# Optimization experiments

Measured on AMD Instinct MI355X. Metric: run time of the kernel, lower is better.

Reference implementation:

```python
import jax, jax.numpy as jnp
import numpy as np

EPS = 1e-5


def bin_act(x):
    # forward of Binaryactivation: sign (STE backward handled in fwdbwd module)
    return jnp.sign(x)


def bin_conv(x, w, stride, padding):
    # per-output-filter scaling factor = mean |w| over (in, kh, kw), detached
    scale = jax.lax.stop_gradient(jnp.mean(jnp.abs(w), axis=(1, 2, 3), keepdims=True))
    bw = scale * jnp.sign(w)
    rw = jnp.clip(w, -1.0, 1.0)
    # STE blend: forward uses binary weight, backward flows through clamp(w)
    filt = jax.lax.stop_gradient(bw - rw) + rw
    return jax.lax.conv_general_dilated(
        x, filt, window_strides=(stride, stride),
        padding=[(padding, padding), (padding, padding)],
        dimension_numbers=("NCHW", "OIHW", "NCHW"))


def batchnorm(x, gamma, beta):
    # training-mode BN: biased batch stats over (N, H, W)
    mean = jnp.mean(x, axis=(0, 2, 3), keepdims=True)
    var = jnp.mean((x - mean) ** 2, axis=(0, 2, 3), keepdims=True)
    xn = (x - mean) * jax.lax.rsqrt(var + EPS)
    return xn * gamma[None, :, None, None] + beta[None, :, None, None]


def prelu(x, a):
    a = a[None, :, None, None]
    return jnp.where(x >= 0, x, a * x)


def addbias(x, b):
    return x + b[None, :, None, None]


def setup_inputs() -> dict:
    key = jax.random.key(0)
    ks = jax.random.split(key, 4)
    C = 256
    x = jax.random.normal(ks[0], (32, C, 56, 56), dtype=jnp.float32)
    # BinaryConv weights init: uniform[0, 0.001)
    w3x3 = jax.random.uniform(ks[1], (C, C, 3, 3), dtype=jnp.float32) * 0.001
    wres = jax.random.uniform(ks[2], (C, C, 1, 1), dtype=jnp.float32) * 0.001
    zeros = jnp.zeros((C,), dtype=jnp.float32)
    ones = jnp.ones((C,), dtype=jnp.float32)
    prelu_init = jnp.full((C,), 0.25, dtype=jnp.float32)
    return {
        "x": x,
        "b1_1": zeros, "w3x3": w3x3, "bn1_g": ones, "bn1_b": zeros,
        "b1_2": zeros, "prelu1_a": prelu_init, "b1_3": zeros,
        "b2_1": zeros, "wres": wres, "bn2_g": ones, "bn2_b": zeros,
        "b2_2": zeros, "prelu2_a": prelu_init, "b2_3": zeros,
    }


def reference(x, b1_1, w3x3, bn1_g, bn1_b, b1_2, prelu1_a, b1_3,
              b2_1, wres, bn2_g, bn2_b, b2_2, prelu2_a, b2_3):
    # branch 1: bias -> sign -> binary 3x3 conv -> BN -> residual add
    x1 = bin_act(addbias(x, b1_1))
    x1 = bin_conv(x1, w3x3, stride=1, padding=1)
    x1 = batchnorm(x1, bn1_g, bn1_b)
    x = x + x1
    x = addbias(x, b1_2)
    x = prelu(x, prelu1_a)
    x = addbias(x, b1_3)
    # branch 2 (in_channel == out_channel): binary 1x1 conv residual
    x2 = bin_act(addbias(x, b2_1))
    x2 = bin_conv(x2, wres, stride=1, padding=0)
    x2 = batchnorm(x2, bn2_g, bn2_b)
    x2 = x2 + x
    x2 = addbias(x2, b2_2)
    x2 = prelu(x2, prelu2_a)
    x2 = addbias(x2, b2_3)
    return x2
```

## Files before the change

### kernel.cpp

```cpp
#include <hip/hip_runtime.h>
#include <cstdint>
#include <math.h>

#define HW    3136
#define NPIX  100352
#define NELEM 25690112

#define OFF_PW1   0u
#define OFF_PW2   73728u
#define OFF_CORR  81920u
#define OFF_SC1   86016u
#define OFF_SC2   87040u
#define OFF_A1    88064u
#define OFF_B1    89088u
#define OFF_A2    90112u
#define OFF_B2    91136u
#define OFF_ST    92160u
#define ST_BYTES  524288u
#define OFF_P1    616448u
#define OFF_P2    3827712u
#define OFF_S1    7038976u
#define OFF_S2    58419200u

__global__ __launch_bounds__(256) void prep_w_k(const float* __restrict__ w3,
                         const float* __restrict__ wr,
                         uint32_t* __restrict__ pw1, uint32_t* __restrict__ pw2,
                         float* __restrict__ sc1, float* __restrict__ sc2,
                         short* __restrict__ corrG) {
  __shared__ float s1S[4], s2S[4];
  __shared__ int cntS[9][4];
  const int o = blockIdx.x;
  const int tid = threadIdx.x;
  const int l = tid & 63, wv = tid >> 6;
  const float* wo = w3 + (size_t)o * 2304 + (size_t)tid * 9;
  float w9[9];
#pragma unroll
  for (int t = 0; t < 9; ++t) w9[t] = wo[t];
  float s = 0.f;
#pragma unroll
  for (int t = 0; t < 9; ++t) s += fabsf(w9[t]);
#pragma unroll
  for (int m = 32; m; m >>= 1) s += __shfl_xor(s, m, 64);
#pragma unroll
  for (int t = 0; t < 9; ++t) {
    unsigned long long mb = __ballot(w9[t] >= 0.0f);
    if (l == 0) {
      pw1[(size_t)(o * 9 + t) * 8 + wv * 2 + 0] = (uint32_t)mb;
      pw1[(size_t)(o * 9 + t) * 8 + wv * 2 + 1] = (uint32_t)(mb >> 32);
      cntS[t][wv] = __popcll(mb);
    }
  }
  float v2 = wr[(size_t)o * 256 + tid];
  float s2 = fabsf(v2);
#pragma unroll
  for (int m = 32; m; m >>= 1) s2 += __shfl_xor(s2, m, 64);
  unsigned long long mb2 = __ballot(v2 >= 0.0f);
  if (l == 0) {
    pw2[(size_t)o * 8 + wv * 2 + 0] = (uint32_t)mb2;
    pw2[(size_t)o * 8 + wv * 2 + 1] = (uint32_t)(mb2 >> 32);
    s1S[wv] = s; s2S[wv] = s2;
  }
  __syncthreads();
  if (tid == 0) {
    sc1[o] = (s1S[0] + s1S[1] + s1S[2] + s1S[3]) / 2304.0f;
    sc2[o] = (s2S[0] + s2S[1] + s2S[2] + s2S[3]) / 256.0f;
    int wsum[9];
#pragma unroll
    for (int t = 0; t < 9; ++t)
      wsum[t] = 2 * (cntS[t][0] + cntS[t][1] + cntS[t][2] + cntS[t][3]) - 256;
    corrG[o * 8 + 0] = (short)(wsum[0] + wsum[1] + wsum[2]);
    corrG[o * 8 + 1] = (short)(wsum[6] + wsum[7] + wsum[8]);
    corrG[o * 8 + 2] = (short)(wsum[0] + wsum[3] + wsum[6]);
    corrG[o * 8 + 3] = (short)(wsum[2] + wsum[5] + wsum[8]);
    corrG[o * 8 + 4] = (short)wsum[0];
    corrG[o * 8 + 5] = (short)wsum[2];
    corrG[o * 8 + 6] = (short)wsum[6];
    corrG[o * 8 + 7] = (short)wsum[8];
  }
}

__global__ __launch_bounds__(256) void pack1_k(const float* __restrict__ x,
                                               const float* __restrict__ b1_1,
                                               uint32_t* __restrict__ p1) {
  const int j = blockIdx.y;
  const int gpx = blockIdx.x * 256 + threadIdx.x;
  const int n = gpx / 784;
  const int p4 = (gpx - n * 784) * 4;
  const float* xb = x + ((size_t)n * 256 + j * 32) * HW + p4;
  uint32_t w0 = 0, w1 = 0, w2 = 0, w3 = 0;
#pragma unroll
  for (int cc = 0; cc < 32; ++cc) {
    float4 v = *(const float4*)(xb + (size_t)cc * HW);
    float bb = b1_1[j * 32 + cc];
    w0 |= (v.x + bb >= 0.f) ? (1u << cc) : 0u;
    w1 |= (v.y + bb >= 0.f) ? (1u << cc) : 0u;
    w2 |= (v.z + bb >= 0.f) ? (1u << cc) : 0u;
    w3 |= (v.w + bb >= 0.f) ? (1u << cc) : 0u;
  }
  uint4 o = {w0, w1, w2, w3};
  *(uint4*)&p1[(size_t)j * NPIX + gpx * 4] = o;
}

__global__ __launch_bounds__(256, 4) void conv1_k(const uint32_t* __restrict__ p1,
    const uint32_t* __restrict__ pw1, const short* __restrict__ corrG,
    short* __restrict__ S1, unsigned long long* __restrict__ st1) {
  __shared__ __align__(16) uint32_t actS[840];
  __shared__ __align__(16) uint32_t wtS[9216];
  const int tid = threadIdx.x;
  const int bx = blockIdx.x;
  const int ty = bx / 7, tx = bx % 7;
  const int n = blockIdx.y;
  const int zh = blockIdx.z;
  const int h0 = ty * 8 - 1, w0 = tx * 8 - 1;
  for (int i = tid; i < 800; i += 256) {
    int r = i / 80, cq = i % 80;
    int c = cq >> 3;
    int hh = h0 + r, ww = w0 + c;
    uint32_t v = 0;
    if ((unsigned)hh < 56u && (unsigned)ww < 56u)
      v = p1[(size_t)(cq & 7) * NPIX + (size_t)n * HW + hh * 56 + ww];
    actS[r * 84 + cq] = v;
  }
  const uint32_t* pwB = pw1 + (size_t)zh * 9216;
  for (int i = tid; i < 2304; i += 256)
    ((uint4*)wtS)[i] = ((const uint4*)pwB)[i];
  __syncthreads();

  const int pr = tid & 7;
  const int chg = tid >> 3;
  const uint32_t* wp = wtS + chg * 72;

  int acc[4][8];
#pragma unroll
  for (int j = 0; j < 4; ++j)
#pragma unroll
    for (int k = 0; k < 8; ++k) acc[j][k] = 0;

#pragma unroll 1
  for (int dh = 0; dh < 3; ++dh) {
#pragma unroll 1
    for (int q4 = 0; q4 < 2; ++q4) {
      uint4 a10[10];
      const uint32_t* ar = actS + (pr + dh) * 84 + q4 * 4;
#pragma unroll
      for (int c2 = 0; c2 < 10; ++c2) a10[c2] = *(const uint4*)(ar + c2 * 8);
#pragma unroll
      for (int j = 0; j < 4; ++j) {
        const uint32_t* wj = wp + j * 2304 + q4 * 4 + dh * 24;
        uint4 wA = *(const uint4*)(wj + 0);
        uint4 wB = *(const uint4*)(wj + 8);
        uint4 wC = *(const uint4*)(wj + 16);
#pragma unroll
        for (int k = 0; k < 8; ++k) {
          uint4 a0 = a10[k];
          uint4 a1 = a10[k + 1];
          uint4 a2 = a10[k + 2];
          int t = acc[j][k];
          t += __builtin_popcount(a0.x ^ wA.x);
          t += __builtin_popcount(a0.y ^ wA.y);
          t += __builtin_popcount(a0.z ^ wA.z);
          t += __builtin_popcount(a0.w ^ wA.w);
          t += __builtin_popcount(a1.x ^ wB.x);
          t += __builtin_popcount(a1.y ^ wB.y);
          t += __builtin_popcount(a1.z ^ wB.z);
          t += __builtin_popcount(a1.w ^ wB.w);
          t += __builtin_popcount(a2.x ^ wC.x);
          t += __builtin_popcount(a2.y ^ wC.y);
          t += __builtin_popcount(a2.z ^ wC.z);
          t += __builtin_popcount(a2.w ^ wC.w);
          acc[j][k] = t;
        }
      }
    }
  }

  const int h = ty * 8 + pr;
  const bool hT = (h == 0), hB = (h == 55);
  const int slot = (bx + n * 49) & 63;
#pragma unroll
  for (int j = 0; j < 4; ++j) {
    const int ch_l = chg + 32 * j;
    short c8[8];
    *(int4*)c8 = *(const int4*)(corrG + (size_t)(zh * 128 + ch_l) * 8);
    int cH = hT ? (int)c8[0] : (hB ? (int)c8[1] : 0);
    int s[8];
#pragma unroll
    for (int k = 0; k < 8; ++k) s[k] = 2304 - 2 * acc[j][k] + cH;
    if (tx == 0) s[0] += (int)c8[2] - (hT ? (int)c8[4] : (hB ? (int)c8[6] : 0));
    if (tx == 6) s[7] += (int)c8[3] - (hT ? (int)c8[5] : (hB ? (int)c8[7] : 0));
    int sm = 0, sq = 0;
#pragma unroll
    for (int k = 0; k < 8; ++k) { sm += s[k]; sq += s[k] * s[k]; }
    uint4 val;
    val.x = (uint32_t)(uint16_t)s[0] | ((uint32_t)(uint16_t)s[1] << 16);
    val.y = (uint32_t)(uint16_t)s[2] | ((uint32_t)(uint16_t)s[3] << 16);
    val.z = (uint32_t)(uint16_t)s[4] | ((uint32_t)(uint16_t)s[5] << 16);
    val.w = (uint32_t)(uint16_t)s[6] | ((uint32_t)(uint16_t)s[7] << 16);
    *(uint4*)&S1[(((size_t)n * 49 + bx) * 256 + zh * 128 + ch_l) * 64 + pr * 8] = val;
#pragma unroll
    for (int m = 1; m < 8; m <<= 1) { sm += __shfl_xor(sm, m, 64); sq += __shfl_xor(sq, m, 64); }
    if (pr == 0) {
      unsigned long long* st = st1 + ((size_t)(zh * 128 + ch_l) * 64 + slot) * 2;
      atomicAdd(&st[0], (unsigned long long)(long long)sm);
      atomicAdd(&st[1], (unsigned long long)(long long)sq);
    }
  }
}

__global__ void bnfin_k(const unsigned long long* __restrict__ st, const float* __restrict__ sc,
                        const float* __restrict__ g, const float* __restrict__ b,
                        float* __restrict__ A, float* __restrict__ B) {
  const int c = blockIdx.x, l = threadIdx.x;
  long long sm = (long long)st[((size_t)c * 64 + l) * 2 + 0];
  long long sq = (long long)st[((size_t)c * 64 + l) * 2 + 1];
  for (int m = 1; m < 64; m <<= 1) { sm += __shfl_xor(sm, m, 64); sq += __shfl_xor(sq, m, 64); }
  if (l == 0) {
    const double M = (double)NPIX;
    double mS = (double)sm / M;
    double vS = (double)sq / M - mS * mS;
    double scale = (double)sc[c];
    double mean = scale * mS;
    double var = scale * scale * vS;
    double rstd = 1.0 / sqrt(var + 1e-5);
    double gd = (double)g[c];
    A[c] = (float)(gd * scale * rstd);
    B[c] = (float)((double)b[c] - gd * mean * rstd);
  }
}

__global__ __launch_bounds__(256) void pack2_k(const float* __restrict__ x,
    const short* __restrict__ S1,
    const float* __restrict__ A1, const float* __restrict__ B1,
    const float* __restrict__ b1_2, const float* __restrict__ a1,
    const float* __restrict__ b1_3, const float* __restrict__ b2_1,
    uint32_t* __restrict__ p2) {
  const int j = blockIdx.y;
  const int gpx = blockIdx.x * 256 + threadIdx.x;
  const int n = gpx / 784;
  const int p4 = (gpx - n * 784) * 4;
  const int h = p4 / 56, w = p4 - (p4 / 56) * 56;
  const int tile = (h >> 3) * 7 + (w >> 3);
  const int px = (h & 7) * 8 + (w & 7);
  const float* xb = x + ((size_t)n * 256 + j * 32) * HW + p4;
  const short* s1b = S1 + (((size_t)n * 49 + tile) * 256 + j * 32) * 64 + px;
  uint32_t w0 = 0, w1 = 0, w2 = 0, w3 = 0;
#pragma unroll
  for (int cc = 0; cc < 32; ++cc) {
    int c = j * 32 + cc;
    float4 xv = *(const float4*)(xb + (size_t)cc * HW);
    short4 s1 = *(const short4*)(s1b + cc * 64);
    float Ac = A1[c], Bc = B1[c], p12 = b1_2[c], al = a1[c], p13 = b1_3[c], p21 = b2_1[c];
    float u, v, t;
    u = xv.x + (Ac * (float)s1.x + Bc) + p12; v = u >= 0.f ? u : al * u; t = v + p13 + p21;
    w0 |= (t >= 0.f) ? (1u << cc) : 0u;
    u = xv.y + (Ac * (float)s1.y + Bc) + p12; v = u >= 0.f ? u : al * u; t = v + p13 + p21;
    w1 |= (t >= 0.f) ? (1u << cc) : 0u;
    u = xv.z + (Ac * (float)s1.z + Bc) + p12; v = u >= 0.f ? u : al * u; t = v + p13 + p21;
    w2 |= (t >= 0.f) ? (1u << cc) : 0u;
    u = xv.w + (Ac * (float)s1.w + Bc) + p12; v = u >= 0.f ? u : al * u; t = v + p13 + p21;
    w3 |= (t >= 0.f) ? (1u << cc) : 0u;
  }
  uint4 o = {w0, w1, w2, w3};
  *(uint4*)&p2[(size_t)j * NPIX + gpx * 4] = o;
}

__global__ __launch_bounds__(256) void conv2_k(const uint32_t* __restrict__ p2,
                                               const uint32_t* __restrict__ pw2,
                                               short* __restrict__ S2,
                                               unsigned long long* __restrict__ st2) {
  __shared__ __align__(16) uint32_t actS[512];
  __shared__ __align__(16) uint32_t wtS[1024];
  const int tid = threadIdx.x;
  const int bx = blockIdx.x;
  const int zh = blockIdx.y;
  const int pg0 = bx * 64;
  for (int i = tid; i < 512; i += 256) {
    int gq = i >> 2, ws_ = i & 3;
    int pxl = gq >> 1, q4 = gq & 1;
    int q = q4 * 4 + ws_;
    actS[((gq ^ ((gq >> 3) & 15)) << 2) + ws_] = p2[q * NPIX + pg0 + pxl];
  }
  if (tid < 256)
    ((uint4*)wtS)[tid] = ((const uint4*)(pw2 + zh * 1024))[tid];
  __syncthreads();
  const int pxg = tid & 15, chg = tid >> 4;
  int acc[8][4];
#pragma unroll
  for (int j = 0; j < 8; ++j)
#pragma unroll
    for (int k = 0; k < 4; ++k) acc[j][k] = 0;
#pragma unroll
  for (int q4 = 0; q4 < 2; ++q4) {
    uint4 a[4];
#pragma unroll
    for (int k = 0; k < 4; ++k) {
      int gq = 8 * pxg + 2 * k + q4;
      a[k] = *(const uint4*)&actS[(gq ^ pxg) << 2];
    }
#pragma unroll
    for (int j = 0; j < 8; ++j) {
      uint4 w = *(const uint4*)&wtS[(chg + 16 * j) * 8 + q4 * 4];
#pragma unroll
      for (int k = 0; k < 4; ++k) {
        int t = acc[j][k];
        t += __builtin_popcount(a[k].x ^ w.x);
        t += __builtin_popcount(a[k].y ^ w.y);
        t += __builtin_popcount(a[k].z ^ w.z);
        t += __builtin_popcount(a[k].w ^ w.w);
        acc[j][k] = t;
      }
    }
  }
  const int slot = bx & 63;
#pragma unroll
  for (int j = 0; j < 8; ++j) {
    const int c_l = chg + 16 * j;
    int s[4], sm = 0, sq = 0;
#pragma unroll
    for (int k = 0; k < 4; ++k) {
      s[k] = 256 - 2 * acc[j][k];
      sm += s[k]; sq += s[k] * s[k];
    }
    short4 o4;
    o4.x = (short)s[0]; o4.y = (short)s[1]; o4.z = (short)s[2]; o4.w = (short)s[3];
    *(short4*)&S2[(((size_t)bx * 256) + zh * 128 + c_l) * 64 + pxg * 4] = o4;
#pragma unroll
    for (int m = 1; m < 16; m <<= 1) { sm += __shfl_xor(sm, m, 64); sq += __shfl_xor(sq, m, 64); }
    if (pxg == 0) {
      unsigned long long* st = st2 + ((size_t)(zh * 128 + c_l) * 64 + slot) * 2;
      atomicAdd(&st[0], (unsigned long long)(long long)sm);
      atomicAdd(&st[1], (unsigned long long)(long long)sq);
    }
  }
}

__global__ __launch_bounds__(256) void final_k(const float* __restrict__ x,
    const short* __restrict__ S1, const short* __restrict__ S2,
    const float* __restrict__ A1, const float* __restrict__ B1,
    const float* __restrict__ b1_2, const float* __restrict__ a1, const float* __restrict__ b1_3,
    const float* __restrict__ A2, const float* __restrict__ B2,
    const float* __restrict__ b2_2, const float* __restrict__ a2, const float* __restrict__ b2_3,
    float* __restrict__ out) {
  const int gi = blockIdx.x * 256 + threadIdx.x;
  const int i4 = gi * 4;
  const int nc = i4 / 3136;
  const int p = i4 - nc * 3136;
  const int n = nc >> 8, c = nc & 255;
  const int h = p / 56, w = p - (p / 56) * 56;
  const int tile = (h >> 3) * 7 + (w >> 3);
  const int px = (h & 7) * 8 + (w & 7);
  short4 s1 = *(const short4*)&S1[(((size_t)n * 49 + tile) * 256 + c) * 64 + px];
  const int pg = n * 3136 + p;
  short4 s2 = *(const short4*)&S2[((size_t)(pg >> 6) * 256 + c) * 64 + (pg & 63)];
  float4 xv = *(const float4*)&x[i4];
  const float A1c = A1[c], B1c = B1[c], P12 = b1_2[c], AL1 = a1[c], P13 = b1_3[c];
  const float A2c = A2[c], B2c = B2[c], P22 = b2_2[c], AL2 = a2[c], P23 = b2_3[c];
  float xs[4] = {xv.x, xv.y, xv.z, xv.w};
  float f1[4] = {(float)s1.x, (float)s1.y, (float)s1.z, (float)s1.w};
  float f2[4] = {(float)s2.x, (float)s2.y, (float)s2.z, (float)s2.w};
  float o[4];
#pragma unroll
  for (int e = 0; e < 4; ++e) {
    float u = xs[e] + (A1c * f1[e] + B1c);
    u = u + P12;
    float v = u >= 0.0f ? u : AL1 * u;
    float t = v + P13;
    float z = (A2c * f2[e] + B2c) + t;
    z = z + P22;
    float vv = z >= 0.0f ? z : AL2 * z;
    o[e] = vv + P23;
  }
  float4 ov = {o[0], o[1], o[2], o[3]};
  *(float4*)&out[i4] = ov;
}

extern "C" void kernel_launch(void* const* d_in, const int* in_sizes, int n_in,
                              void* d_out, int out_size, void* d_ws, size_t ws_size,
                              hipStream_t stream) {
  const float* x    = (const float*)d_in[0];
  const float* b1_1 = (const float*)d_in[1];
  const float* w3x3 = (const float*)d_in[2];
  const float* bn1g = (const float*)d_in[3];
  const float* bn1b = (const float*)d_in[4];
  const float* b1_2 = (const float*)d_in[5];
  const float* a1   = (const float*)d_in[6];
  const float* b1_3 = (const float*)d_in[7];
  const float* b2_1 = (const float*)d_in[8];
  const float* wres = (const float*)d_in[9];
  const float* bn2g = (const float*)d_in[10];
  const float* bn2b = (const float*)d_in[11];
  const float* b2_2 = (const float*)d_in[12];
  const float* a2   = (const float*)d_in[13];
  const float* b2_3 = (const float*)d_in[14];

  char* ws = (char*)d_ws;
  uint32_t* pw1 = (uint32_t*)(ws + OFF_PW1);
  uint32_t* pw2 = (uint32_t*)(ws + OFF_PW2);
  short* corrG = (short*)(ws + OFF_CORR);
  float* sc1 = (float*)(ws + OFF_SC1);
  float* sc2 = (float*)(ws + OFF_SC2);
  float* A1 = (float*)(ws + OFF_A1);
  float* B1 = (float*)(ws + OFF_B1);
  float* A2 = (float*)(ws + OFF_A2);
  float* B2 = (float*)(ws + OFF_B2);
  unsigned long long* st1 = (unsigned long long*)(ws + OFF_ST);
  unsigned long long* st2 = (unsigned long long*)(ws + OFF_ST + 262144u);
  uint32_t* p1 = (uint32_t*)(ws + OFF_P1);
  uint32_t* p2 = (uint32_t*)(ws + OFF_P2);
  short* S1 = (short*)(ws + OFF_S1);
  short* S2 = (short*)(ws + OFF_S2);

  hipMemsetAsync(ws + OFF_ST, 0, ST_BYTES, stream);
  prep_w_k<<<256, 256, 0, stream>>>(w3x3, wres, pw1, pw2, sc1, sc2, corrG);
  pack1_k<<<dim3(98, 8), 256, 0, stream>>>(x, b1_1, p1);
  conv1_k<<<dim3(49, 32, 2), 256, 0, stream>>>(p1, pw1, corrG, S1, st1);
  bnfin_k<<<256, 64, 0, stream>>>(st1, sc1, bn1g, bn1b, A1, B1);
  pack2_k<<<dim3(98, 8), 256, 0, stream>>>(x, S1, A1, B1, b1_2, a1, b1_3, b2_1, p2);
  conv2_k<<<dim3(1568, 2), 256, 0, stream>>>(p2, pw2, S2, st2);
  bnfin_k<<<256, 64, 0, stream>>>(st2, sc2, bn2g, bn2b, A2, B2);
  final_k<<<25088, 256, 0, stream>>>(x, S1, S2, A1, B1, b1_2, a1, b1_3,
                                     A2, B2, b2_2, a2, b2_3, (float*)d_out);
}
```

Baseline: 477.2 us.

## Replace XOR-popcount 3x3 binary conv with int8 MFMA using ±1 bytes

Result: slower. 575.3 us (+20.6%).

```diff
diff --git a/kernel.cpp b/kernel.cpp
--- a/kernel.cpp
+++ b/kernel.cpp
@@ -22,34 +22,22 @@
 #define OFF_S1    7038976u
 #define OFF_S2    58419200u
 
+typedef int i32x4 __attribute__((ext_vector_type(4)));
+
 __global__ __launch_bounds__(256) void prep_w_k(const float* __restrict__ w3,
                          const float* __restrict__ wr,
-                         uint32_t* __restrict__ pw1, uint32_t* __restrict__ pw2,
-                         float* __restrict__ sc1, float* __restrict__ sc2,
-                         short* __restrict__ corrG) {
+                         uint32_t* __restrict__ pw2,
+                         float* __restrict__ sc1, float* __restrict__ sc2) {
   __shared__ float s1S[4], s2S[4];
-  __shared__ int cntS[9][4];
   const int o = blockIdx.x;
   const int tid = threadIdx.x;
   const int l = tid & 63, wv = tid >> 6;
   const float* wo = w3 + (size_t)o * 2304 + (size_t)tid * 9;
-  float w9[9];
-#pragma unroll
-  for (int t = 0; t < 9; ++t) w9[t] = wo[t];
   float s = 0.f;
 #pragma unroll
-  for (int t = 0; t < 9; ++t) s += fabsf(w9[t]);
+  for (int t = 0; t < 9; ++t) s += fabsf(wo[t]);
 #pragma unroll
   for (int m = 32; m; m >>= 1) s += __shfl_xor(s, m, 64);
-#pragma unroll
-  for (int t = 0; t < 9; ++t) {
-    unsigned long long mb = __ballot(w9[t] >= 0.0f);
-    if (l == 0) {
-      pw1[(size_t)(o * 9 + t) * 8 + wv * 2 + 0] = (uint32_t)mb;
-      pw1[(size_t)(o * 9 + t) * 8 + wv * 2 + 1] = (uint32_t)(mb >> 32);
-      cntS[t][wv] = __popcll(mb);
-    }
-  }
   float v2 = wr[(size_t)o * 256 + tid];
   float s2 = fabsf(v2);
 #pragma unroll
@@ -64,143 +52,147 @@
   if (tid == 0) {
     sc1[o] = (s1S[0] + s1S[1] + s1S[2] + s1S[3]) / 2304.0f;
     sc2[o] = (s2S[0] + s2S[1] + s2S[2] + s2S[3]) / 256.0f;
-    int wsum[9];
-#pragma unroll
-    for (int t = 0; t < 9; ++t)
-      wsum[t] = 2 * (cntS[t][0] + cntS[t][1] + cntS[t][2] + cntS[t][3]) - 256;
-    corrG[o * 8 + 0] = (short)(wsum[0] + wsum[1] + wsum[2]);
-    corrG[o * 8 + 1] = (short)(wsum[6] + wsum[7] + wsum[8]);
-    corrG[o * 8 + 2] = (short)(wsum[0] + wsum[3] + wsum[6]);
-    corrG[o * 8 + 3] = (short)(wsum[2] + wsum[5] + wsum[8]);
-    corrG[o * 8 + 4] = (short)wsum[0];
-    corrG[o * 8 + 5] = (short)wsum[2];
-    corrG[o * 8 + 6] = (short)wsum[6];
-    corrG[o * 8 + 7] = (short)wsum[8];
-  }
-}
-
-__global__ __launch_bounds__(256) void pack1_k(const float* __restrict__ x,
-                                               const float* __restrict__ b1_1,
-                                               uint32_t* __restrict__ p1) {
-  const int j = blockIdx.y;
-  const int gpx = blockIdx.x * 256 + threadIdx.x;
-  const int n = gpx / 784;
-  const int p4 = (gpx - n * 784) * 4;
-  const float* xb = x + ((size_t)n * 256 + j * 32) * HW + p4;
-  uint32_t w0 = 0, w1 = 0, w2 = 0, w3 = 0;
-#pragma unroll
-  for (int cc = 0; cc < 32; ++cc) {
-    float4 v = *(const float4*)(xb + (size_t)cc * HW);
-    float bb = b1_1[j * 32 + cc];
-    w0 |= (v.x + bb >= 0.f) ? (1u << cc) : 0u;
-    w1 |= (v.y + bb >= 0.f) ? (1u << cc) : 0u;
-    w2 |= (v.z + bb >= 0.f) ? (1u << cc) : 0u;
-    w3 |= (v.w + bb >= 0.f) ? (1u << cc) : 0u;
-  }
-  uint4 o = {w0, w1, w2, w3};
-  *(uint4*)&p1[(size_t)j * NPIX + gpx * 4] = o;
-}
-
-__global__ __launch_bounds__(256, 4) void conv1_k(const uint32_t* __restrict__ p1,
-    const uint32_t* __restrict__ pw1, const short* __restrict__ corrG,
-    short* __restrict__ S1, unsigned long long* __restrict__ st1) {
-  __shared__ __align__(16) uint32_t actS[840];
-  __shared__ __align__(16) uint32_t wtS[9216];
+  }
+}
+
+__global__ void prep_wfrag_k(const float* __restrict__ w3, char* __restrict__ wf) {
+  const int s = blockIdx.x, t = blockIdx.y;
+  const int l = threadIdx.x;
+  const int och = t * 16 + (l & 15), lg = l >> 4;
+  const int tap = s >> 2;
+  const int chb = (s & 3) * 64 + lg * 16;
+  const float* wp = w3 + (size_t)och * 2304 + tap;
+  uint32_t wd[4];
+#pragma unroll
+  for (int u = 0; u < 4; ++u) {
+    uint32_t v = 0;
+#pragma unroll
+    for (int i = 0; i < 4; ++i) {
+      float x = wp[(size_t)(chb + u * 4 + i) * 9];
+      uint32_t b = (x >= 0.f) ? 0x01u : 0xFFu;
+      v |= b << (8 * i);
+    }
+    wd[u] = v;
+  }
+  uint4 o; o.x = wd[0]; o.y = wd[1]; o.z = wd[2]; o.w = wd[3];
+  *(uint4*)&wf[((size_t)(s * 16 + t) * 64 + l) * 16] = o;
+}
+
+__global__ __launch_bounds__(256) void pack_act_k(const float* __restrict__ x,
+                                                  const float* __restrict__ b1_1,
+                                                  char* __restrict__ act) {
+  const int gid = blockIdx.x * 256 + threadIdx.x;
+  const int pxid = gid >> 1, half = gid & 1;
+  const int n = pxid / 3136, p = pxid - n * 3136;
+  const float* xb = x + ((size_t)n * 256 + half * 128) * 3136 + p;
+  const float* bb = b1_1 + half * 128;
+  uint32_t w[32];
+#pragma unroll
+  for (int cc = 0; cc < 128; ++cc) {
+    float v = xb[(size_t)cc * 3136] + bb[cc];
+    uint32_t b = (v >= 0.f) ? 0x01u : 0xFFu;
+    if ((cc & 3) == 0) w[cc >> 2] = b;
+    else               w[cc >> 2] |= b << ((cc & 3) * 8);
+  }
+  uint4* dst = (uint4*)&act[(size_t)pxid * 256 + half * 128];
+#pragma unroll
+  for (int u = 0; u < 8; ++u) {
+    uint4 o; o.x = w[u*4]; o.y = w[u*4+1]; o.z = w[u*4+2]; o.w = w[u*4+3];
+    dst[u] = o;
+  }
+}
+
+__global__ __launch_bounds__(256, 2) void conv1_k(const char* __restrict__ act,
+    const char* __restrict__ wf, short* __restrict__ S1,
+    unsigned long long* __restrict__ st1) {
+  __shared__ __align__(16) char actS[25600];
+  __shared__ __align__(16) char wS[2][16384];
   const int tid = threadIdx.x;
-  const int bx = blockIdx.x;
+  const int bx = blockIdx.x, n = blockIdx.y;
   const int ty = bx / 7, tx = bx % 7;
-  const int n = blockIdx.y;
-  const int zh = blockIdx.z;
+  const int lane = tid & 63, wv = tid >> 6;
   const int h0 = ty * 8 - 1, w0 = tx * 8 - 1;
-  for (int i = tid; i < 800; i += 256) {
-    int r = i / 80, cq = i % 80;
-    int c = cq >> 3;
+  const char* actB = act + (size_t)n * 3136 * 256;
+  for (int i = tid; i < 1600; i += 256) {
+    int cell = i >> 4, ck = i & 15;
+    int r = cell / 10, c = cell - r * 10;
     int hh = h0 + r, ww = w0 + c;
-    uint32_t v = 0;
+    uint4 v; v.x = 0; v.y = 0; v.z = 0; v.w = 0;
     if ((unsigned)hh < 56u && (unsigned)ww < 56u)
-      v = p1[(size_t)(cq & 7) * NPIX + (size_t)n * HW + hh * 56 + ww];
-    actS[r * 84 + cq] = v;
-  }
-  const uint32_t* pwB = pw1 + (size_t)zh * 9216;
-  for (int i = tid; i < 2304; i += 256)
-    ((uint4*)wtS)[i] = ((const uint4*)pwB)[i];
+      v = *(const uint4*)(actB + (size_t)(hh * 56 + ww) * 256 + ck * 16);
+    *(uint4*)&actS[cell * 256 + (ck ^ (cell & 7)) * 16] = v;
+  }
+  uint4 wreg[4];
+  {
+    const uint4* src = (const uint4*)wf;
+#pragma unroll
+    for (int u = 0; u < 4; ++u) wreg[u] = src[tid * 4 + u];
+    uint4* dst = (uint4*)&wS[0][0];
+#pragma unroll
+    for (int u = 0; u < 4; ++u) dst[tid * 4 + u] = wreg[u];
+  }
   __syncthreads();
 
-  const int pr = tid & 7;
-  const int chg = tid >> 3;
-  const uint32_t* wp = wtS + chg * 72;
-
-  int acc[4][8];
-#pragma unroll
-  for (int j = 0; j < 4; ++j)
-#pragma unroll
-    for (int k = 0; k < 8; ++k) acc[j][k] = 0;
+  i32x4 C[4][4];
+#pragma unroll
+  for (int m = 0; m < 4; ++m)
+#pragma unroll
+    for (int tt = 0; tt < 4; ++tt) C[m][tt] = (i32x4){0, 0, 0, 0};
 
 #pragma unroll 1
-  for (int dh = 0; dh < 3; ++dh) {
-#pragma unroll 1
-    for (int q4 = 0; q4 < 2; ++q4) {
-      uint4 a10[10];
-      const uint32_t* ar = actS + (pr + dh) * 84 + q4 * 4;
-#pragma unroll
-      for (int c2 = 0; c2 < 10; ++c2) a10[c2] = *(const uint4*)(ar + c2 * 8);
-#pragma unroll
-      for (int j = 0; j < 4; ++j) {
-        const uint32_t* wj = wp + j * 2304 + q4 * 4 + dh * 24;
-        uint4 wA = *(const uint4*)(wj + 0);
-        uint4 wB = *(const uint4*)(wj + 8);
-        uint4 wC = *(const uint4*)(wj + 16);
-#pragma unroll
-        for (int k = 0; k < 8; ++k) {
-          uint4 a0 = a10[k];
-          uint4 a1 = a10[k + 1];
-          uint4 a2 = a10[k + 2];
-          int t = acc[j][k];
-          t += __builtin_popcount(a0.x ^ wA.x);
-          t += __builtin_popcount(a0.y ^ wA.y);
-          t += __builtin_popcount(a0.z ^ wA.z);
-          t += __builtin_popcount(a0.w ^ wA.w);
-          t += __builtin_popcount(a1.x ^ wB.x);
-          t += __builtin_popcount(a1.y ^ wB.y);
-          t += __builtin_popcount(a1.z ^ wB.z);
-          t += __builtin_popcount(a1.w ^ wB.w);
-          t += __builtin_popcount(a2.x ^ wC.x);
-          t += __builtin_popcount(a2.y ^ wC.y);
-          t += __builtin_popcount(a2.z ^ wC.z);
-          t += __builtin_popcount(a2.w ^ wC.w);
-          acc[j][k] = t;
-        }
-      }
-    }
-  }
-
-  const int h = ty * 8 + pr;
-  const bool hT = (h == 0), hB = (h == 55);
+  for (int s = 0; s < 36; ++s) {
+    const int b = s & 1;
+    if (s < 35) {
+      const uint4* src = (const uint4*)(wf + (size_t)(s + 1) * 16384);
+#pragma unroll
+      for (int u = 0; u < 4; ++u) wreg[u] = src[tid * 4 + u];
+    }
+    const int tap = s >> 2, chq = s & 3;
+    const int dh = tap / 3, dw = tap - dh * 3;
+    i32x4 Af[4];
+#pragma unroll
+    for (int m = 0; m < 4; ++m) {
+      int pxl = m * 16 + (lane & 15);
+      int cell = ((pxl >> 3) + dh) * 10 + (pxl & 7) + dw;
+      int ck = (chq * 4 + (lane >> 4)) ^ (cell & 7);
+      Af[m] = *(const i32x4*)&actS[cell * 256 + ck * 16];
+    }
+    i32x4 Bf[4];
+#pragma unroll
+    for (int tt = 0; tt < 4; ++tt)
+      Bf[tt] = *(const i32x4*)&wS[b][((wv * 4 + tt) * 64 + lane) * 16];
+#pragma unroll
+    for (int m = 0; m < 4; ++m)
+#pragma unroll
+      for (int tt = 0; tt < 4; ++tt)
+        C[m][tt] = __builtin_amdgcn_mfma_i32_16x16x64_i8(Af[m], Bf[tt], C[m][tt], 0, 0, 0);
+    if (s < 35) {
+      uint4* dst = (uint4*)&wS[b ^ 1][0];
+#pragma unroll
+      for (int u = 0; u < 4; ++u) dst[tid * 4 + u] = wreg[u];
+    }
+    __syncthreads();
+  }
+
   const int slot = (bx + n * 49) & 63;
-#pragma unroll
-  for (int j = 0; j < 4; ++j) {
-    const int ch_l = chg + 32 * j;
-    short c8[8];
-    *(int4*)c8 = *(const int4*)(corrG + (size_t)(zh * 128 + ch_l) * 8);
-    int cH = hT ? (int)c8[0] : (hB ? (int)c8[1] : 0);
-    int s[8];
-#pragma unroll
-    for (int k = 0; k < 8; ++k) s[k] = 2304 - 2 * acc[j][k] + cH;
-    if (tx == 0) s[0] += (int)c8[2] - (hT ? (int)c8[4] : (hB ? (int)c8[6] : 0));
-    if (tx == 6) s[7] += (int)c8[3] - (hT ? (int)c8[5] : (hB ? (int)c8[7] : 0));
+  const size_t s1base = ((size_t)n * 49 + bx) * 256;
+#pragma unroll
+  for (int tt = 0; tt < 4; ++tt) {
+    const int och = (wv * 4 + tt) * 16 + (lane & 15);
     int sm = 0, sq = 0;
 #pragma unroll
-    for (int k = 0; k < 8; ++k) { sm += s[k]; sq += s[k] * s[k]; }
-    uint4 val;
-    val.x = (uint32_t)(uint16_t)s[0] | ((uint32_t)(uint16_t)s[1] << 16);
-    val.y = (uint32_t)(uint16_t)s[2] | ((uint32_t)(uint16_t)s[3] << 16);
-    val.z = (uint32_t)(uint16_t)s[4] | ((uint32_t)(uint16_t)s[5] << 16);
-    val.w = (uint32_t)(uint16_t)s[6] | ((uint32_t)(uint16_t)s[7] << 16);
-    *(uint4*)&S1[(((size_t)n * 49 + bx) * 256 + zh * 128 + ch_l) * 64 + pr * 8] = val;
-#pragma unroll
-    for (int m = 1; m < 8; m <<= 1) { sm += __shfl_xor(sm, m, 64); sq += __shfl_xor(sq, m, 64); }
-    if (pr == 0) {
-      unsigned long long* st = st1 + ((size_t)(zh * 128 + ch_l) * 64 + slot) * 2;
+    for (int m = 0; m < 4; ++m) {
+      i32x4 v = C[m][tt];
+      short4 o4;
+      o4.x = (short)v.x; o4.y = (short)v.y; o4.z = (short)v.z; o4.w = (short)v.w;
+      *(short4*)&S1[(s1base + och) * 64 + m * 16 + (lane >> 4) * 4] = o4;
+      sm += v.x + v.y + v.z + v.w;
+      sq += v.x * v.x + v.y * v.y + v.z * v.z + v.w * v.w;
+    }
+    sm += __shfl_xor(sm, 16, 64); sm += __shfl_xor(sm, 32, 64);
+    sq += __shfl_xor(sq, 16, 64); sq += __shfl_xor(sq, 32, 64);
+    if (lane < 16) {
+      unsigned long long* st = st1 + ((size_t)och * 64 + slot) * 2;
       atomicAdd(&st[0], (unsigned long long)(long long)sm);
       atomicAdd(&st[1], (unsigned long long)(long long)sq);
     }
@@ -394,9 +386,7 @@
   const float* b2_3 = (const float*)d_in[14];
 
   char* ws = (char*)d_ws;
-  uint32_t* pw1 = (uint32_t*)(ws + OFF_PW1);
   uint32_t* pw2 = (uint32_t*)(ws + OFF_PW2);
-  short* corrG = (short*)(ws + OFF_CORR);
   float* sc1 = (float*)(ws + OFF_SC1);
   float* sc2 = (float*)(ws + OFF_SC2);
   float* A1 = (float*)(ws + OFF_A1);
@@ -405,15 +395,17 @@
   float* B2 = (float*)(ws + OFF_B2);
   unsigned long long* st1 = (unsigned long long*)(ws + OFF_ST);
   unsigned long long* st2 = (unsigned long long*)(ws + OFF_ST + 262144u);
-  uint32_t* p1 = (uint32_t*)(ws + OFF_P1);
+  char* wf  = (char*)(ws + OFF_P1);
   uint32_t* p2 = (uint32_t*)(ws + OFF_P2);
   short* S1 = (short*)(ws + OFF_S1);
   short* S2 = (short*)(ws + OFF_S2);
+  char* act = (char*)(ws + OFF_S2);
 
   hipMemsetAsync(ws + OFF_ST, 0, ST_BYTES, stream);
-  prep_w_k<<<256, 256, 0, stream>>>(w3x3, wres, pw1, pw2, sc1, sc2, corrG);
-  pack1_k<<<dim3(98, 8), 256, 0, stream>>>(x, b1_1, p1);
-  conv1_k<<<dim3(49, 32, 2), 256, 0, stream>>>(p1, pw1, corrG, S1, st1);
+  prep_w_k<<<256, 256, 0, stream>>>(w3x3, wres, pw2, sc1, sc2);
+  prep_wfrag_k<<<dim3(36, 16), 64, 0, stream>>>(w3x3, wf);
+  pack_act_k<<<784, 256, 0, stream>>>(x, b1_1, act);
+  conv1_k<<<dim3(49, 32), 256, 0, stream>>>(act, wf, S1, st1);
   bnfin_k<<<256, 64, 0, stream>>>(st1, sc1, bn1g, bn1b, A1, B1);
   pack2_k<<<dim3(98, 8), 256, 0, stream>>>(x, S1, A1, B1, b1_2, a1, b1_3, b2_1, p2);
   conv2_k<<<dim3(1568, 2), 256, 0, stream>>>(p2, pw2, S2, st2);
```
